# Optimization experiments

Measured on AMD Instinct MI355X. Metric: run time of the kernel, lower is better.

The kernel has to match this reference:

```python
import jax, jax.numpy as jnp
import numpy as np

N_TOK = 384          # sentence length n
SEQ = N_TOK + 2      # + START, STOP
H = 256              # lstm_dim (per-direction hidden)
EMB = 128            # tag_embedding_dim == word_embedding_dim (embeddings are summed)
TAGV, WORDV, LABV = 64, 10000, 128
LABH = SPLH = 256


def _lstm_dir(x, Wx, Wh, b, reverse=False):
    # x: [S, EMB]; Wx: [4H, EMB]; Wh: [4H, H]; b: [4H]. PyTorch gate order i,f,g,o.
    Hdim = Wh.shape[1]

    def cell(carry, xt):
        h, c = carry
        g = Wx @ xt + Wh @ h + b
        i, f, gg, o = jnp.split(g, 4)
        c = jax.nn.sigmoid(f) * c + jax.nn.sigmoid(i) * jnp.tanh(gg)
        h = jax.nn.sigmoid(o) * jnp.tanh(c)
        return (h, c), h

    init = (jnp.zeros((Hdim,), x.dtype), jnp.zeros((Hdim,), x.dtype))
    _, hs = jax.lax.scan(cell, init, x, reverse=reverse)
    return hs  # [S, H]


def _mlp(x, w1, b1, w2, b2):
    return jnp.maximum(x @ w1.T + b1, 0.0) @ w2.T + b2


def setup_inputs() -> dict:
    key = jax.random.key(0)
    ks = jax.random.split(key, 18)
    s = 0.05
    return {
        'tag_ids': jax.random.randint(ks[0], (SEQ,), 0, TAGV, dtype=jnp.int32),
        'word_ids': jax.random.randint(ks[1], (SEQ,), 0, WORDV, dtype=jnp.int32),
        'tag_emb': jax.random.normal(ks[2], (TAGV, EMB), jnp.float32) * s,
        'word_emb': jax.random.normal(ks[3], (WORDV, EMB), jnp.float32) * s,
        'wxf': jax.random.normal(ks[4], (4 * H, EMB), jnp.float32) * s,
        'whf': jax.random.normal(ks[5], (4 * H, H), jnp.float32) * s,
        'bf': jax.random.normal(ks[6], (4 * H,), jnp.float32) * s,
        'wxb': jax.random.normal(ks[7], (4 * H, EMB), jnp.float32) * s,
        'whb': jax.random.normal(ks[8], (4 * H, H), jnp.float32) * s,
        'bb': jax.random.normal(ks[9], (4 * H,), jnp.float32) * s,
        'lab_w1': jax.random.normal(ks[10], (LABH, 2 * H), jnp.float32) * s,
        'lab_b1': jax.random.normal(ks[11], (LABH,), jnp.float32) * s,
        'lab_w2': jax.random.normal(ks[12], (LABV, LABH), jnp.float32) * s,
        'lab_b2': jax.random.normal(ks[13], (LABV,), jnp.float32) * s,
        'spl_w1': jax.random.normal(ks[14], (SPLH, 2 * H), jnp.float32) * s,
        'spl_b1': jax.random.normal(ks[15], (SPLH,), jnp.float32) * s,
        'spl_w2': jax.random.normal(ks[16], (1, SPLH), jnp.float32) * s,
        'spl_b2': jax.random.normal(ks[17], (1,), jnp.float32) * s,
    }


def reference(tag_ids, word_ids, tag_emb, word_emb, wxf, whf, bf, wxb, whb, bb,
              lab_w1, lab_b1, lab_w2, lab_b2, spl_w1, spl_b1, spl_w2, spl_b2):
    n = tag_ids.shape[0] - 2
    # token embeddings: tag + word (as in parse())
    emb = tag_emb[tag_ids] + word_emb[word_ids]            # [S, EMB]
    hf = _lstm_dir(emb, wxf, whf, bf, reverse=False)        # [S, H] forward dir
    hb = _lstm_dir(emb, wxb, whb, bb, reverse=True)         # [S, H] backward dir
    # span encoding for every (left, right), 0 <= left,right <= n:
    #   fwd = hf[right] - hf[left];  bwd = hb[left+1] - hb[right+1]
    f = hf[: n + 1]                                         # [n+1, H]
    b1 = hb[1 : n + 2]                                      # [n+1, H]
    enc_f = f[None, :, :] - f[:, None, :]                   # [l, r, H]
    enc_b = b1[:, None, :] - b1[None, :, :]                 # [l, r, H]
    enc = jnp.concatenate([enc_f, enc_b], axis=-1)          # [n+1, n+1, 2H]
    # batched f_label / f_split over the whole chart
    label_scores = _mlp(enc, lab_w1, lab_b1, lab_w2, lab_b2)  # [n+1, n+1, LABV]
    split_scores = _mlp(enc, spl_w1, spl_b1, spl_w2, spl_b2)  # [n+1, n+1, 1]
    return jnp.concatenate([label_scores, split_scores], axis=-1)  # [n+1, n+1, LABV+1]
```

## Files before the change

kernel.cpp:

```cpp
#include <hip/hip_runtime.h>
#include <cstdint>

#define SEQ   386
#define NP1   385
#define HDIM  256
#define G4    1024
#define EMBD  128
#define LABV  128
#define OUTC  129

typedef _Float16 h2 __attribute__((ext_vector_type(2)));
typedef _Float16 f16x8 __attribute__((ext_vector_type(8)));
typedef float    f32x4 __attribute__((ext_vector_type(4)));

__device__ __forceinline__ uint32_t pack2(float a, float b) {
    h2 v; v[0] = (_Float16)a; v[1] = (_Float16)b;
    return __builtin_bit_cast(uint32_t, v);
}

__device__ __forceinline__ float dot2(uint32_t wa, uint32_t hb, float c) {
    h2 a = __builtin_bit_cast(h2, wa);
    h2 b = __builtin_bit_cast(h2, hb);
#if __has_builtin(__builtin_amdgcn_fdot2)
    return __builtin_amdgcn_fdot2(a, b, c, false);
#else
    return fmaf((float)a[1], (float)b[1], fmaf((float)a[0], (float)b[0], c));
#endif
}

__device__ __forceinline__ float sigm(float x) { return 1.f / (1.f + __expf(-x)); }
__device__ __forceinline__ float ftanh(float x) {
    x = fminf(fmaxf(x, -15.f), 15.f);
    float e = __expf(2.f * x);
    return (e - 1.f) / (e + 1.f);
}

#define OFF_EMB   0u
#define OFF_GX    197632u
#define OFF_WREG  3359744u
#define OFF_WLDS  4146176u
#define OFF_F     4408320u
#define OFF_B     4802560u
#define OFF_DL    5196800u
#define OFF_DS    5591040u
#define OFF_W2F   5985280u

__global__ void k_embed(const int* __restrict__ tag_ids, const int* __restrict__ word_ids,
                        const float* __restrict__ tag_emb, const float* __restrict__ word_emb,
                        float* __restrict__ emb) {
    int t = blockIdx.x, d = threadIdx.x;
    emb[t * EMBD + d] = tag_emb[tag_ids[t] * EMBD + d] + word_emb[word_ids[t] * EMBD + d];
}

__global__ __launch_bounds__(256) void k_gx(const float* __restrict__ emb,
                                            const float* __restrict__ wxf, const float* __restrict__ bf_,
                                            const float* __restrict__ wxb, const float* __restrict__ bb_,
                                            float* __restrict__ gx) {
    const int dir = blockIdx.y;
    const int t0  = blockIdx.x * 8;
    const float* Wx   = dir ? wxb : wxf;
    const float* bias = dir ? bb_ : bf_;
    __shared__ float se[8 * EMBD];
    for (int idx = threadIdx.x; idx < 8 * EMBD; idx += 256) {
        int tt = t0 + (idx >> 7);
        se[idx] = (tt < SEQ) ? emb[tt * EMBD + (idx & 127)] : 0.f;
    }
    __syncthreads();
    const float4* se4 = (const float4*)se;
    for (int q = 0; q < 4; ++q) {
        int r = threadIdx.x + q * 256;
        float bv = bias[r];
        float acc[8];
#pragma unroll
        for (int tt = 0; tt < 8; ++tt) acc[tt] = bv;
        const float4* wrow = (const float4*)(Wx + r * EMBD);
        for (int d4 = 0; d4 < 32; ++d4) {
            float4 w = wrow[d4];
#pragma unroll
            for (int tt = 0; tt < 8; ++tt) {
                float4 e = se4[tt * 32 + d4];
                acc[tt] += w.x * e.x + w.y * e.y + w.z * e.z + w.w * e.w;
            }
        }
        for (int tt = 0; tt < 8; ++tt) {
            int t = t0 + tt;
            if (t < SEQ) gx[(dir * SEQ + t) * G4 + r] = acc[tt];
        }
    }
}

__global__ void k_wconv(const float* __restrict__ whf, const float* __restrict__ whb,
                        uint4* __restrict__ wreg, uint32_t* __restrict__ wlds) {
    const int dir = blockIdx.x;
    const float* Wh = dir ? whb : whf;
    const int y = blockIdx.y, tid = threadIdx.x;
    if (y < 96) {
        int idx = y * 256 + tid;
        int r = idx / 24, cg = idx % 24;
        const float* src = Wh + r * HDIM + cg * 8;
        uint4 o;
        o.x = pack2(src[0], src[1]); o.y = pack2(src[2], src[3]);
        o.z = pack2(src[4], src[5]); o.w = pack2(src[6], src[7]);
        wreg[dir * 24576 + cg * 1024 + r] = o;
    } else {
        int idx = (y - 96) * 256 + tid;
        int r = idx >> 5, c = idx & 31;
        wlds[dir * 32768 + r * 32 + c] = pack2(Wh[r * HDIM + 192 + 2 * c], Wh[r * HDIM + 193 + 2 * c]);
    }
}

__global__ __launch_bounds__(512)
__attribute__((amdgpu_waves_per_eu(2, 2)))
void k_lstm(const uint4* __restrict__ wreg,
            const uint32_t* __restrict__ wlds,
            const float* __restrict__ gx,
            float* __restrict__ fout, float* __restrict__ bout) {
    const int dir = blockIdx.x;
    const int tid = threadIdx.x;
    __shared__ uint32_t wl[1024 * 36];
    __shared__ float gbuf[1024];
    __shared__ __align__(16) uint32_t hsh[136];

    const uint32_t* wsrc = wlds + dir * 32768;
    for (int idx = tid; idx < 32768; idx += 512)
        wl[(idx >> 5) * 36 + (idx & 31)] = wsrc[idx];
    if (tid < 136) hsh[tid] = 0u;

    uint4 w0[24], w1[24];
    const uint4* wr = wreg + dir * 24576;
#pragma unroll
    for (int g = 0; g < 24; ++g) {
        w0[g] = wr[g * 1024 + tid];
        w1[g] = wr[g * 1024 + tid + 512];
    }

    const float* gxd = gx + dir * SEQ * G4;
    float c = 0.f;
    const int tfirst = dir ? (SEQ - 1) : 0;
    float gxv0 = gxd[tfirst * G4 + tid];
    float gxv1 = gxd[tfirst * G4 + tid + 512];
    __syncthreads();

    const uint4* h4 = (const uint4*)hsh;
    const uint4* wlr0 = (const uint4*)(wl + tid * 36);
    const uint4* wlr1 = (const uint4*)(wl + (tid + 512) * 36);

    for (int s = 0; s < SEQ; ++s) {
        int t = dir ? (SEQ - 1 - s) : s;
        float gn0 = 0.f, gn1 = 0.f;
        if (s < SEQ - 1) {
            int tn = dir ? (SEQ - 2 - s) : (s + 1);
            gn0 = gxd[tn * G4 + tid];
            gn1 = gxd[tn * G4 + tid + 512];
        }
        float a0 = gxv0, a1 = gxv1;
#pragma unroll
        for (int g = 0; g < 24; ++g) {
            uint4 hv = h4[g];
            a0 = dot2(w0[g].x, hv.x, a0);
            a0 = dot2(w0[g].y, hv.y, a0);
            a0 = dot2(w0[g].z, hv.z, a0);
            a0 = dot2(w0[g].w, hv.w, a0);
            a1 = dot2(w1[g].x, hv.x, a1);
            a1 = dot2(w1[g].y, hv.y, a1);
            a1 = dot2(w1[g].z, hv.z, a1);
            a1 = dot2(w1[g].w, hv.w, a1);
        }
#pragma unroll
        for (int g = 0; g < 8; ++g) {
            uint4 hv = h4[24 + g];
            uint4 v0 = wlr0[g];
            uint4 v1 = wlr1[g];
            a0 = dot2(v0.x, hv.x, a0);
            a0 = dot2(v0.y, hv.y, a0);
            a0 = dot2(v0.z, hv.z, a0);
            a0 = dot2(v0.w, hv.w, a0);
            a1 = dot2(v1.x, hv.x, a1);
            a1 = dot2(v1.y, hv.y, a1);
            a1 = dot2(v1.z, hv.z, a1);
            a1 = dot2(v1.w, hv.w, a1);
        }
        gbuf[tid] = a0;
        gbuf[tid + 512] = a1;
        __syncthreads();
        if (tid < HDIM) {
            float gi = gbuf[tid];
            float gf = gbuf[tid + 256];
            float gg = gbuf[tid + 512];
            float go = gbuf[tid + 768];
            c = sigm(gf) * c + sigm(gi) * ftanh(gg);
            float h = sigm(go) * ftanh(c);
            ((_Float16*)hsh)[tid] = (_Float16)h;
            if (!dir) { if (t < NP1) fout[t * HDIM + tid] = h; }
            else      { if (t >= 1)  bout[(t - 1) * HDIM + tid] = h; }
        }
        __syncthreads();
        gxv0 = gn0;
        gxv1 = gn1;
    }
}

__global__ __launch_bounds__(256) void k_dmat(const float* __restrict__ fm, const float* __restrict__ bm,
                                              const float* __restrict__ lw1, const float* __restrict__ sw1,
                                              float* __restrict__ dlab, float* __restrict__ dspl) {
    const int t0 = blockIdx.x * 8;
    const int tid = threadIdx.x;
    __shared__ float fs[8 * HDIM], bs[8 * HDIM];
    for (int idx = tid; idx < 8 * HDIM; idx += 256) {
        int tt = t0 + (idx >> 8);
        float fv = 0.f, bv = 0.f;
        if (tt < NP1) { fv = fm[tt * HDIM + (idx & 255)]; bv = bm[tt * HDIM + (idx & 255)]; }
        fs[idx] = fv; bs[idx] = bv;
    }
    __syncthreads();
    float al[8], asp[8];
#pragma unroll
    for (int q = 0; q < 8; ++q) { al[q] = 0.f; asp[q] = 0.f; }
    const float4* lrow = (const float4*)(lw1 + tid * 512);
    const float4* srow = (const float4*)(sw1 + tid * 512);
    const float4* fs4 = (const float4*)fs;
    const float4* bs4 = (const float4*)bs;
    for (int d4 = 0; d4 < 64; ++d4) {
        float4 wlv = lrow[d4], wsv = srow[d4];
#pragma unroll
        for (int tt = 0; tt < 8; ++tt) {
            float4 e = fs4[tt * 64 + d4];
            al[tt]  += wlv.x * e.x + wlv.y * e.y + wlv.z * e.z + wlv.w * e.w;
            asp[tt] += wsv.x * e.x + wsv.y * e.y + wsv.z * e.z + wsv.w * e.w;
        }
    }
    for (int d4 = 0; d4 < 64; ++d4) {
        float4 wlv = lrow[64 + d4], wsv = srow[64 + d4];
#pragma unroll
        for (int tt = 0; tt < 8; ++tt) {
            float4 e = bs4[tt * 64 + d4];
            al[tt]  -= wlv.x * e.x + wlv.y * e.y + wlv.z * e.z + wlv.w * e.w;
            asp[tt] -= wsv.x * e.x + wsv.y * e.y + wsv.z * e.z + wsv.w * e.w;
        }
    }
    for (int tt = 0; tt < 8; ++tt) {
        int t = t0 + tt;
        if (t < NP1) { dlab[t * HDIM + tid] = al[tt]; dspl[t * HDIM + tid] = asp[tt]; }
    }
}

__global__ void k_w2f(const float* __restrict__ lw2, _Float16* __restrict__ w2f) {
    int m = blockIdx.x, k = threadIdx.x;
    w2f[(((k >> 3) * LABV) + m) * 8 + (k & 7)] = (_Float16)lw2[m * HDIM + k];
}

__global__ __launch_bounds__(256) void k_out(const float* __restrict__ dlab, const float* __restrict__ dspl,
                                             const float* __restrict__ lb1, const float* __restrict__ sb1,
                                             const _Float16* __restrict__ w2f, const float* __restrict__ lb2,
                                             const float* __restrict__ sw2, const float* __restrict__ sb2,
                                             float* __restrict__ outp) {
    const int i = blockIdx.y, jtblk = blockIdx.x, tid = threadIdx.x;
    __shared__ float dli[HDIM], dsi[HDIM];
    __shared__ _Float16 hl[32 * 264];

    dli[tid] = dlab[i * HDIM + tid] - lb1[tid];
    dsi[tid] = dspl[i * HDIM + tid] - sb1[tid];
    __syncthreads();

    for (int j = 0; j < 32; ++j) {
        int jj = jtblk * 32 + j;
        float v = 0.f;
        if (jj < NP1) v = fmaxf(dlab[jj * HDIM + tid] - dli[tid], 0.f);
        hl[j * 264 + tid] = (_Float16)v;
    }

    {
        int w = tid >> 6, l = tid & 63;
        float sw2v[4];
#pragma unroll
        for (int cc = 0; cc < 4; ++cc) sw2v[cc] = sw2[l + 64 * cc];
        float sb2v = sb2[0];
        for (int q = 0; q < 8; ++q) {
            int jj = jtblk * 32 + w * 8 + q;
            if (jj < NP1) {
                float sum = 0.f;
#pragma unroll
                for (int cc = 0; cc < 4; ++cc) {
                    int k = l + 64 * cc;
                    float v = fmaxf(dspl[jj * HDIM + k] - dsi[k], 0.f);
                    sum += v * sw2v[cc];
                }
#pragma unroll
                for (int off = 32; off > 0; off >>= 1) sum += __shfl_down(sum, off, 64);
                if (l == 0) outp[(size_t)(i * NP1 + jj) * OUTC + 128] = sum + sb2v;
            }
        }
    }
    __syncthreads();

    const int w = tid >> 6, l = tid & 63;
    const int q = l >> 4, c16 = l & 15;
    f32x4 acc[2][2];
#pragma unroll
    for (int a = 0; a < 2; ++a)
#pragma unroll
        for (int b = 0; b < 2; ++b) acc[a][b] = (f32x4){0.f, 0.f, 0.f, 0.f};

    const int mt0 = w * 2;
#pragma unroll
    for (int kb = 0; kb < 8; ++kb) {
        f16x8 a0 = *(const f16x8*)(hl + (0 * 16 + c16) * 264 + kb * 32 + q * 8);
        f16x8 a1 = *(const f16x8*)(hl + (1 * 16 + c16) * 264 + kb * 32 + q * 8);
        f16x8 b0 = *(const f16x8*)(w2f + (((kb * 4 + q) * LABV) + mt0 * 16 + c16) * 8);
        f16x8 b1 = *(const f16x8*)(w2f + (((kb * 4 + q) * LABV) + (mt0 + 1) * 16 + c16) * 8);
        acc[0][0] = __builtin_amdgcn_mfma_f32_16x16x32_f16(a0, b0, acc[0][0], 0, 0, 0);
        acc[0][1] = __builtin_amdgcn_mfma_f32_16x16x32_f16(a0, b1, acc[0][1], 0, 0, 0);
        acc[1][0] = __builtin_amdgcn_mfma_f32_16x16x32_f16(a1, b0, acc[1][0], 0, 0, 0);
        acc[1][1] = __builtin_amdgcn_mfma_f32_16x16x32_f16(a1, b1, acc[1][1], 0, 0, 0);
    }

#pragma unroll
    for (int mb = 0; mb < 2; ++mb) {
        int m = (mt0 + mb) * 16 + c16;
        float bias = lb2[m];
#pragma unroll
        for (int jt = 0; jt < 2; ++jt) {
#pragma unroll
            for (int r = 0; r < 4; ++r) {
                int jj = jtblk * 32 + jt * 16 + q * 4 + r;
                if (jj < NP1) outp[(size_t)(i * NP1 + jj) * OUTC + m] = acc[jt][mb][r] + bias;
            }
        }
    }
}

extern "C" void kernel_launch(void* const* d_in, const int* in_sizes, int n_in,
                              void* d_out, int out_size, void* d_ws, size_t ws_size,
                              hipStream_t stream) {
    const int*   tag_ids  = (const int*)d_in[0];
    const int*   word_ids = (const int*)d_in[1];
    const float* tag_emb  = (const float*)d_in[2];
    const float* word_emb = (const float*)d_in[3];
    const float* wxf = (const float*)d_in[4];
    const float* whf = (const float*)d_in[5];
    const float* bf_ = (const float*)d_in[6];
    const float* wxb = (const float*)d_in[7];
    const float* whb = (const float*)d_in[8];
    const float* bb_ = (const float*)d_in[9];
    const float* lw1 = (const float*)d_in[10];
    const float* lb1 = (const float*)d_in[11];
    const float* lw2 = (const float*)d_in[12];
    const float* lb2 = (const float*)d_in[13];
    const float* sw1 = (const float*)d_in[14];
    const float* sb1 = (const float*)d_in[15];
    const float* sw2 = (const float*)d_in[16];
    const float* sb2 = (const float*)d_in[17];

    char* ws = (char*)d_ws;
    float*     emb  = (float*)(ws + OFF_EMB);
    float*     gx   = (float*)(ws + OFF_GX);
    uint4*     wreg = (uint4*)(ws + OFF_WREG);
    uint32_t*  wlds = (uint32_t*)(ws + OFF_WLDS);
    float*     fm   = (float*)(ws + OFF_F);
    float*     bm   = (float*)(ws + OFF_B);
    float*     dlab = (float*)(ws + OFF_DL);
    float*     dspl = (float*)(ws + OFF_DS);
    _Float16*  w2f  = (_Float16*)(ws + OFF_W2F);
    float*     outp = (float*)d_out;

    k_embed<<<dim3(SEQ), dim3(EMBD), 0, stream>>>(tag_ids, word_ids, tag_emb, word_emb, emb);
    k_gx   <<<dim3(49, 2), dim3(256), 0, stream>>>(emb, wxf, bf_, wxb, bb_, gx);
    k_wconv<<<dim3(2, 224), dim3(256), 0, stream>>>(whf, whb, wreg, wlds);
    k_w2f  <<<dim3(LABV), dim3(HDIM), 0, stream>>>(lw2, w2f);
    k_lstm <<<dim3(2), dim3(512), 0, stream>>>(wreg, wlds, gx, fm, bm);
    k_dmat <<<dim3(49), dim3(256), 0, stream>>>(fm, bm, lw1, sw1, dlab, dspl);
    k_out  <<<dim3(13, NP1), dim3(256), 0, stream>>>(dlab, dspl, lb1, sb1, w2f, lb2, sw2, sb2, outp);
}
```

Before: 892.3 us.

## Compute all four gates per thread in LSTM to drop gate-exchange barrier

Remaps the recurrent LSTM kernel so each of 256 threads owns one hidden unit and computes all four gate rows (i,f,g,o) itself, holding 96 uint4 of fp16 weights in registers. This removes the shared gate buffer and one of the two block barriers per timestep, and double-buffers the hidden state so only one sync is needed. The weight-conversion kernel is reordered to match the new register layout. The trade-off is fewer waves per step (one wave per SIMD), much higher register pressure with possible spills, and four times the serial dot work per thread.

```diff
diff --git a/kernel.cpp b/kernel.cpp
--- a/kernel.cpp
+++ b/kernel.cpp
@@ -96,12 +96,15 @@
     const int y = blockIdx.y, tid = threadIdx.x;
     if (y < 96) {
         int idx = y * 256 + tid;
-        int r = idx / 24, cg = idx % 24;
-        const float* src = Wh + r * HDIM + cg * 8;
+        int tidd = idx & 255;
+        int qg = idx >> 8;
+        int q = qg / 24, g = qg % 24;
+        int r = tidd + 256 * q;
+        const float* src = Wh + r * HDIM + g * 8;
         uint4 o;
         o.x = pack2(src[0], src[1]); o.y = pack2(src[2], src[3]);
         o.z = pack2(src[4], src[5]); o.w = pack2(src[6], src[7]);
-        wreg[dir * 24576 + cg * 1024 + r] = o;
+        wreg[dir * 24576 + idx] = o;
     } else {
         int idx = (y - 96) * 256 + tid;
         int r = idx >> 5, c = idx & 31;
@@ -109,8 +112,8 @@
     }
 }
 
-__global__ __launch_bounds__(512)
-__attribute__((amdgpu_waves_per_eu(2, 2)))
+__global__ __launch_bounds__(256, 1)
+__attribute__((amdgpu_waves_per_eu(1, 1)))
 void k_lstm(const uint4* __restrict__ wreg,
             const uint32_t* __restrict__ wlds,
             const float* __restrict__ gx,
@@ -118,85 +121,85 @@
     const int dir = blockIdx.x;
     const int tid = threadIdx.x;
     __shared__ uint32_t wl[1024 * 36];
-    __shared__ float gbuf[1024];
-    __shared__ __align__(16) uint32_t hsh[136];
-
-    const uint32_t* wsrc = wlds + dir * 32768;
-    for (int idx = tid; idx < 32768; idx += 512)
-        wl[(idx >> 5) * 36 + (idx & 31)] = wsrc[idx];
-    if (tid < 136) hsh[tid] = 0u;
-
-    uint4 w0[24], w1[24];
+    __shared__ uint32_t hbuf[2][160];
+
+    const uint4* wsrc4 = (const uint4*)(wlds + dir * 32768);
+    for (int i4 = tid; i4 < 8192; i4 += 256) {
+        uint4 v = wsrc4[i4];
+        *(uint4*)&wl[(i4 >> 3) * 36 + (i4 & 7) * 4] = v;
+    }
+    if (tid < 160) { hbuf[0][tid] = 0u; hbuf[1][tid] = 0u; }
+
+    uint4 w[4][24];
     const uint4* wr = wreg + dir * 24576;
 #pragma unroll
-    for (int g = 0; g < 24; ++g) {
-        w0[g] = wr[g * 1024 + tid];
-        w1[g] = wr[g * 1024 + tid + 512];
-    }
+    for (int q = 0; q < 4; ++q)
+#pragma unroll
+        for (int g = 0; g < 24; ++g)
+            w[q][g] = wr[(q * 24 + g) * 256 + tid];
 
     const float* gxd = gx + dir * SEQ * G4;
     float c = 0.f;
     const int tfirst = dir ? (SEQ - 1) : 0;
-    float gxv0 = gxd[tfirst * G4 + tid];
-    float gxv1 = gxd[tfirst * G4 + tid + 512];
-    __syncthreads();
-
-    const uint4* h4 = (const uint4*)hsh;
-    const uint4* wlr0 = (const uint4*)(wl + tid * 36);
-    const uint4* wlr1 = (const uint4*)(wl + (tid + 512) * 36);
+    float gxv[4], gn[4];
+#pragma unroll
+    for (int q = 0; q < 4; ++q) gxv[q] = gxd[tfirst * G4 + q * 256 + tid];
+
+    const uint4* wlq0 = (const uint4*)(wl + (tid)       * 36);
+    const uint4* wlq1 = (const uint4*)(wl + (tid + 256) * 36);
+    const uint4* wlq2 = (const uint4*)(wl + (tid + 512) * 36);
+    const uint4* wlq3 = (const uint4*)(wl + (tid + 768) * 36);
+    __syncthreads();
 
     for (int s = 0; s < SEQ; ++s) {
-        int t = dir ? (SEQ - 1 - s) : s;
-        float gn0 = 0.f, gn1 = 0.f;
+        const int t = dir ? (SEQ - 1 - s) : s;
         if (s < SEQ - 1) {
             int tn = dir ? (SEQ - 2 - s) : (s + 1);
-            gn0 = gxd[tn * G4 + tid];
-            gn1 = gxd[tn * G4 + tid + 512];
-        }
-        float a0 = gxv0, a1 = gxv1;
+#pragma unroll
+            for (int q = 0; q < 4; ++q) gn[q] = gxd[tn * G4 + q * 256 + tid];
+        } else {
+#pragma unroll
+            for (int q = 0; q < 4; ++q) gn[q] = 0.f;
+        }
+        float a0 = gxv[0], a1 = gxv[1], a2 = gxv[2], a3 = gxv[3];
+        const uint4* hb = (const uint4*)hbuf[s & 1];
+
 #pragma unroll
         for (int g = 0; g < 24; ++g) {
-            uint4 hv = h4[g];
-            a0 = dot2(w0[g].x, hv.x, a0);
-            a0 = dot2(w0[g].y, hv.y, a0);
-            a0 = dot2(w0[g].z, hv.z, a0);
-            a0 = dot2(w0[g].w, hv.w, a0);
-            a1 = dot2(w1[g].x, hv.x, a1);
-            a1 = dot2(w1[g].y, hv.y, a1);
-            a1 = dot2(w1[g].z, hv.z, a1);
-            a1 = dot2(w1[g].w, hv.w, a1);
+            uint4 hv = hb[g];
+            a0 = dot2(w[0][g].x, hv.x, a0); a0 = dot2(w[0][g].y, hv.y, a0);
+            a0 = dot2(w[0][g].z, hv.z, a0); a0 = dot2(w[0][g].w, hv.w, a0);
+            a1 = dot2(w[1][g].x, hv.x, a1); a1 = dot2(w[1][g].y, hv.y, a1);
+            a1 = dot2(w[1][g].z, hv.z, a1); a1 = dot2(w[1][g].w, hv.w, a1);
+            a2 = dot2(w[2][g].x, hv.x, a2); a2 = dot2(w[2][g].y, hv.y, a2);
+            a2 = dot2(w[2][g].z, hv.z, a2); a2 = dot2(w[2][g].w, hv.w, a2);
+            a3 = dot2(w[3][g].x, hv.x, a3); a3 = dot2(w[3][g].y, hv.y, a3);
+            a3 = dot2(w[3][g].z, hv.z, a3); a3 = dot2(w[3][g].w, hv.w, a3);
         }
 #pragma unroll
         for (int g = 0; g < 8; ++g) {
-            uint4 hv = h4[24 + g];
-            uint4 v0 = wlr0[g];
-            uint4 v1 = wlr1[g];
-            a0 = dot2(v0.x, hv.x, a0);
-            a0 = dot2(v0.y, hv.y, a0);
-            a0 = dot2(v0.z, hv.z, a0);
-            a0 = dot2(v0.w, hv.w, a0);
-            a1 = dot2(v1.x, hv.x, a1);
-            a1 = dot2(v1.y, hv.y, a1);
-            a1 = dot2(v1.z, hv.z, a1);
-            a1 = dot2(v1.w, hv.w, a1);
-        }
-        gbuf[tid] = a0;
-        gbuf[tid + 512] = a1;
+            uint4 hv = hb[24 + g];
+            uint4 v0 = wlq0[g];
+            uint4 v1 = wlq1[g];
+            uint4 v2 = wlq2[g];
+            uint4 v3 = wlq3[g];
+            a0 = dot2(v0.x, hv.x, a0); a0 = dot2(v0.y, hv.y, a0);
+            a0 = dot2(v0.z, hv.z, a0); a0 = dot2(v0.w, hv.w, a0);
+            a1 = dot2(v1.x, hv.x, a1); a1 = dot2(v1.y, hv.y, a1);
+            a1 = dot2(v1.z, hv.z, a1); a1 = dot2(v1.w, hv.w, a1);
+            a2 = dot2(v2.x, hv.x, a2); a2 = dot2(v2.y, hv.y, a2);
+            a2 = dot2(v2.z, hv.z, a2); a2 = dot2(v2.w, hv.w, a2);
+            a3 = dot2(v3.x, hv.x, a3); a3 = dot2(v3.y, hv.y, a3);
+            a3 = dot2(v3.z, hv.z, a3); a3 = dot2(v3.w, hv.w, a3);
+        }
+
+        c = sigm(a1) * c + sigm(a0) * ftanh(a2);
+        float h = sigm(a3) * ftanh(c);
+        ((_Float16*)hbuf[(s + 1) & 1])[tid] = (_Float16)h;
+        if (!dir) { if (t < NP1) fout[t * HDIM + tid] = h; }
+        else      { if (t >= 1)  bout[(t - 1) * HDIM + tid] = h; }
         __syncthreads();
-        if (tid < HDIM) {
-            float gi = gbuf[tid];
-            float gf = gbuf[tid + 256];
-            float gg = gbuf[tid + 512];
-            float go = gbuf[tid + 768];
-            c = sigm(gf) * c + sigm(gi) * ftanh(gg);
-            float h = sigm(go) * ftanh(c);
-            ((_Float16*)hsh)[tid] = (_Float16)h;
-            if (!dir) { if (t < NP1) fout[t * HDIM + tid] = h; }
-            else      { if (t >= 1)  bout[(t - 1) * HDIM + tid] = h; }
-        }
-        __syncthreads();
-        gxv0 = gn0;
-        gxv1 = gn1;
+        gxv[0] = gn[0]; gxv[1] = gn[1]; gxv[2] = gn[2]; gxv[3] = gn[3];
     }
 }
 
@@ -367,7 +370,7 @@
     k_gx   <<<dim3(49, 2), dim3(256), 0, stream>>>(emb, wxf, bf_, wxb, bb_, gx);
     k_wconv<<<dim3(2, 224), dim3(256), 0, stream>>>(whf, whb, wreg, wlds);
     k_w2f  <<<dim3(LABV), dim3(HDIM), 0, stream>>>(lw2, w2f);
-    k_lstm <<<dim3(2), dim3(512), 0, stream>>>(wreg, wlds, gx, fm, bm);
+    k_lstm <<<dim3(2), dim3(256), 0, stream>>>(wreg, wlds, gx, fm, bm);
     k_dmat <<<dim3(49), dim3(256), 0, stream>>>(fm, bm, lw1, sw1, dlab, dspl);
     k_out  <<<dim3(13, NP1), dim3(256), 0, stream>>>(dlab, dspl, lb1, sb1, w2f, lb2, sw2, sb2, outp);
 }
```

After: 1.539 ms. 1.72x slower.

## Split each LSTM direction across two workgroups with flag-based hidden-state exchange

Applied to the files above, without the earlier changes.

Each LSTM direction now runs on two workgroups, each owning half of the hidden units, so all recurrent weights fit in registers (32 uint4 per thread) instead of partly in LDS. After every step the workgroups swap their fp16 half of h through global memory, using per-step atomic counter flags and spin-waits; a new kernel zeroes the flags. This removes the LDS weight reads and halves the per-thread dot work, but adds a cross-CU global-memory handshake on every one of the 386 serial steps. It also assumes all four blocks are resident at the same time.

```diff
diff --git a/kernel.cpp b/kernel.cpp
--- a/kernel.cpp
+++ b/kernel.cpp
@@ -37,13 +37,14 @@
 
 #define OFF_EMB   0u
 #define OFF_GX    197632u
-#define OFF_WREG  3359744u
-#define OFF_WLDS  4146176u
+#define OFF_WPK   3359744u
 #define OFF_F     4408320u
 #define OFF_B     4802560u
 #define OFF_DL    5196800u
 #define OFF_DS    5591040u
 #define OFF_W2F   5985280u
+#define OFF_HX    6050816u
+#define OFF_FLG   6052864u
 
 __global__ void k_embed(const int* __restrict__ tag_ids, const int* __restrict__ word_ids,
                         const float* __restrict__ tag_emb, const float* __restrict__ word_emb,
@@ -90,113 +91,107 @@
 }
 
 __global__ void k_wconv(const float* __restrict__ whf, const float* __restrict__ whb,
-                        uint4* __restrict__ wreg, uint32_t* __restrict__ wlds) {
+                        uint4* __restrict__ wpk) {
     const int dir = blockIdx.x;
     const float* Wh = dir ? whb : whf;
-    const int y = blockIdx.y, tid = threadIdx.x;
-    if (y < 96) {
-        int idx = y * 256 + tid;
-        int r = idx / 24, cg = idx % 24;
-        const float* src = Wh + r * HDIM + cg * 8;
-        uint4 o;
-        o.x = pack2(src[0], src[1]); o.y = pack2(src[2], src[3]);
-        o.z = pack2(src[4], src[5]); o.w = pack2(src[6], src[7]);
-        wreg[dir * 24576 + cg * 1024 + r] = o;
-    } else {
-        int idx = (y - 96) * 256 + tid;
-        int r = idx >> 5, c = idx & 31;
-        wlds[dir * 32768 + r * 32 + c] = pack2(Wh[r * HDIM + 192 + 2 * c], Wh[r * HDIM + 193 + 2 * c]);
-    }
+    int idx = blockIdx.y * 256 + threadIdx.x;
+    int tl = idx & 511;
+    int c2 = idx >> 9;
+    int half = c2 >> 5, c = c2 & 31;
+    int r = (tl >> 7) * 256 + half * 128 + (tl & 127);
+    const float* src = Wh + r * HDIM + c * 8;
+    uint4 o;
+    o.x = pack2(src[0], src[1]); o.y = pack2(src[2], src[3]);
+    o.z = pack2(src[4], src[5]); o.w = pack2(src[6], src[7]);
+    wpk[((dir * 2 + half) * 32 + c) * 512 + tl] = o;
+}
+
+__global__ void k_zf(int* __restrict__ flags) {
+    int i = blockIdx.x * 256 + threadIdx.x;
+    if (i < 2 * 2 * SEQ) flags[i] = 0;
 }
 
 __global__ __launch_bounds__(512)
-__attribute__((amdgpu_waves_per_eu(2, 2)))
-void k_lstm(const uint4* __restrict__ wreg,
-            const uint32_t* __restrict__ wlds,
+void k_lstm(const uint4* __restrict__ wpk,
             const float* __restrict__ gx,
+            _Float16* __restrict__ hx16, int* __restrict__ flags,
             float* __restrict__ fout, float* __restrict__ bout) {
-    const int dir = blockIdx.x;
-    const int tid = threadIdx.x;
-    __shared__ uint32_t wl[1024 * 36];
-    __shared__ float gbuf[1024];
-    __shared__ __align__(16) uint32_t hsh[136];
-
-    const uint32_t* wsrc = wlds + dir * 32768;
-    for (int idx = tid; idx < 32768; idx += 512)
-        wl[(idx >> 5) * 36 + (idx & 31)] = wsrc[idx];
-    if (tid < 136) hsh[tid] = 0u;
-
-    uint4 w0[24], w1[24];
-    const uint4* wr = wreg + dir * 24576;
-#pragma unroll
-    for (int g = 0; g < 24; ++g) {
-        w0[g] = wr[g * 1024 + tid];
-        w1[g] = wr[g * 1024 + tid + 512];
-    }
-
+    const int b    = blockIdx.x;
+    const int dir  = b >> 1;
+    const int half = b & 1;
+    const int tid  = threadIdx.x;
+    const int q    = tid >> 7;
+    const int el   = tid & 127;
+    const int E    = half * 128 + el;
+
+    __shared__ uint32_t hsh[128];
+    __shared__ float    gbuf[512];
+
+    uint4 w[32];
+    const uint4* wp = wpk + (dir * 2 + half) * 32 * 512;
+#pragma unroll
+    for (int c = 0; c < 32; ++c) w[c] = wp[c * 512 + tid];
+
+    const int r = q * 256 + half * 128 + el;
     const float* gxd = gx + dir * SEQ * G4;
+    uint32_t* hx32 = (uint32_t*)hx16;
+    const int fOwn = (dir * 2 + half) * SEQ;
+    const int fRem = (dir * 2 + (1 - half)) * SEQ;
+
+    if (tid < 128) hsh[tid] = 0u;
     float c = 0.f;
     const int tfirst = dir ? (SEQ - 1) : 0;
-    float gxv0 = gxd[tfirst * G4 + tid];
-    float gxv1 = gxd[tfirst * G4 + tid + 512];
-    __syncthreads();
-
-    const uint4* h4 = (const uint4*)hsh;
-    const uint4* wlr0 = (const uint4*)(wl + tid * 36);
-    const uint4* wlr1 = (const uint4*)(wl + (tid + 512) * 36);
+    float gxv = gxd[tfirst * G4 + r];
+    float gn;
+    __syncthreads();
 
     for (int s = 0; s < SEQ; ++s) {
-        int t = dir ? (SEQ - 1 - s) : s;
-        float gn0 = 0.f, gn1 = 0.f;
+        const int t = dir ? (SEQ - 1 - s) : s;
         if (s < SEQ - 1) {
             int tn = dir ? (SEQ - 2 - s) : (s + 1);
-            gn0 = gxd[tn * G4 + tid];
-            gn1 = gxd[tn * G4 + tid + 512];
-        }
-        float a0 = gxv0, a1 = gxv1;
-#pragma unroll
-        for (int g = 0; g < 24; ++g) {
+            gn = gxd[tn * G4 + r];
+        } else gn = 0.f;
+
+        float a = gxv;
+        const uint4* h4 = (const uint4*)hsh;
+#pragma unroll
+        for (int g = 0; g < 32; ++g) {
             uint4 hv = h4[g];
-            a0 = dot2(w0[g].x, hv.x, a0);
-            a0 = dot2(w0[g].y, hv.y, a0);
-            a0 = dot2(w0[g].z, hv.z, a0);
-            a0 = dot2(w0[g].w, hv.w, a0);
-            a1 = dot2(w1[g].x, hv.x, a1);
-            a1 = dot2(w1[g].y, hv.y, a1);
-            a1 = dot2(w1[g].z, hv.z, a1);
-            a1 = dot2(w1[g].w, hv.w, a1);
-        }
-#pragma unroll
-        for (int g = 0; g < 8; ++g) {
-            uint4 hv = h4[24 + g];
-            uint4 v0 = wlr0[g];
-            uint4 v1 = wlr1[g];
-            a0 = dot2(v0.x, hv.x, a0);
-            a0 = dot2(v0.y, hv.y, a0);
-            a0 = dot2(v0.z, hv.z, a0);
-            a0 = dot2(v0.w, hv.w, a0);
-            a1 = dot2(v1.x, hv.x, a1);
-            a1 = dot2(v1.y, hv.y, a1);
-            a1 = dot2(v1.z, hv.z, a1);
-            a1 = dot2(v1.w, hv.w, a1);
-        }
-        gbuf[tid] = a0;
-        gbuf[tid + 512] = a1;
+            a = dot2(w[g].x, hv.x, a);
+            a = dot2(w[g].y, hv.y, a);
+            a = dot2(w[g].z, hv.z, a);
+            a = dot2(w[g].w, hv.w, a);
+        }
+        gbuf[tid] = a;
         __syncthreads();
-        if (tid < HDIM) {
-            float gi = gbuf[tid];
-            float gf = gbuf[tid + 256];
-            float gg = gbuf[tid + 512];
-            float go = gbuf[tid + 768];
+
+        if (tid < 128) {
+            float gi = gbuf[el];
+            float gf = gbuf[el + 128];
+            float gg = gbuf[el + 256];
+            float go = gbuf[el + 384];
             c = sigm(gf) * c + sigm(gi) * ftanh(gg);
             float h = sigm(go) * ftanh(c);
-            ((_Float16*)hsh)[tid] = (_Float16)h;
-            if (!dir) { if (t < NP1) fout[t * HDIM + tid] = h; }
-            else      { if (t >= 1)  bout[(t - 1) * HDIM + tid] = h; }
+            _Float16 hh = (_Float16)h;
+            ((_Float16*)hsh)[E] = hh;
+            hx16[dir * 512 + (s & 1) * 256 + E] = hh;
+            __threadfence();
+            atomicAdd(&flags[fOwn + s], 1);
+            if (!dir) { if (t < NP1) fout[t * HDIM + E] = h; }
+            else      { if (t >= 1)  bout[(t - 1) * HDIM + E] = h; }
+        } else if (tid < 192) {
+            int p = tid - 128;
+            while (__hip_atomic_load(&flags[fRem + s], __ATOMIC_ACQUIRE,
+                                     __HIP_MEMORY_SCOPE_AGENT) < 128) {
+                __builtin_amdgcn_s_sleep(1);
+            }
+            uint32_t v = __hip_atomic_load(
+                &hx32[dir * 256 + (s & 1) * 128 + (1 - half) * 64 + p],
+                __ATOMIC_RELAXED, __HIP_MEMORY_SCOPE_AGENT);
+            hsh[(1 - half) * 64 + p] = v;
         }
         __syncthreads();
-        gxv0 = gn0;
-        gxv1 = gn1;
+        gxv = gn;
     }
 }
 
@@ -354,20 +349,22 @@
     char* ws = (char*)d_ws;
     float*     emb  = (float*)(ws + OFF_EMB);
     float*     gx   = (float*)(ws + OFF_GX);
-    uint4*     wreg = (uint4*)(ws + OFF_WREG);
-    uint32_t*  wlds = (uint32_t*)(ws + OFF_WLDS);
+    uint4*     wpk  = (uint4*)(ws + OFF_WPK);
     float*     fm   = (float*)(ws + OFF_F);
     float*     bm   = (float*)(ws + OFF_B);
     float*     dlab = (float*)(ws + OFF_DL);
     float*     dspl = (float*)(ws + OFF_DS);
     _Float16*  w2f  = (_Float16*)(ws + OFF_W2F);
+    _Float16*  hx16 = (_Float16*)(ws + OFF_HX);
+    int*       flg  = (int*)(ws + OFF_FLG);
     float*     outp = (float*)d_out;
 
     k_embed<<<dim3(SEQ), dim3(EMBD), 0, stream>>>(tag_ids, word_ids, tag_emb, word_emb, emb);
     k_gx   <<<dim3(49, 2), dim3(256), 0, stream>>>(emb, wxf, bf_, wxb, bb_, gx);
-    k_wconv<<<dim3(2, 224), dim3(256), 0, stream>>>(whf, whb, wreg, wlds);
+    k_wconv<<<dim3(2, 128), dim3(256), 0, stream>>>(whf, whb, wpk);
     k_w2f  <<<dim3(LABV), dim3(HDIM), 0, stream>>>(lw2, w2f);
-    k_lstm <<<dim3(2), dim3(512), 0, stream>>>(wreg, wlds, gx, fm, bm);
+    k_zf   <<<dim3(7), dim3(256), 0, stream>>>(flg);
+    k_lstm <<<dim3(4), dim3(512), 0, stream>>>(wpk, gx, hx16, flg, fm, bm);
     k_dmat <<<dim3(49), dim3(256), 0, stream>>>(fm, bm, lw1, sw1, dlab, dspl);
     k_out  <<<dim3(13, NP1), dim3(256), 0, stream>>>(dlab, dspl, lb1, sb1, w2f, lb2, sw2, sb2, outp);
 }
```

Measured after the change: 1.435 ms. 60.8% more time.
